# Kernel tuning notes

Measured on AMD Instinct MI355X. Metric: run time of the kernel, lower is better.

The kernel has to match this reference:

```python
import math
import jax
import jax.numpy as jnp
from jax import lax
import numpy as np

SEQ = 1024   # must be a perfect square
BSZ = 16
D = 1024     # embed_dim
NDIM = 2
SIDE = 32    # sqrt(SEQ) == one_side_length
SCALE = float(np.sqrt(1.0 / NDIM))


def setup_inputs() -> dict:
    key = jax.random.key(0)
    ks = jax.random.split(key, 8)
    x = jax.random.normal(ks[0], (SEQ, BSZ, D), dtype=jnp.float32)
    A1 = 0.2 * jax.random.normal(ks[1], (D, NDIM), dtype=jnp.float32)
    A2 = 0.2 * jax.random.normal(ks[2], (D, NDIM), dtype=jnp.float32)
    B1 = 0.2 * jax.random.normal(ks[3], (D, NDIM), dtype=jnp.float32)
    B2 = 0.2 * jax.random.normal(ks[4], (D, NDIM), dtype=jnp.float32)
    C1 = jax.random.normal(ks[5], (D, NDIM), dtype=jnp.float32)
    C2 = jax.random.normal(ks[6], (D, NDIM), dtype=jnp.float32)
    omega = jax.random.normal(ks[7], (D,), dtype=jnp.float32)
    return {"x": x, "A1": A1, "A2": A2, "B1": B1, "B2": B2,
            "C1": C1, "C2": C2, "omega": omega}


def _compute_kernel(A1, A2, B1, B2, C1, C2, n):
    """2D SSM impulse-response kernel K: (D, n, n).

    Recurrence (same math the coeff-matrix path-sum in compute_x_matrix encodes,
    cf. one_step):
      h[i,j] = a1*h[i,j-1] + a2*v[i,j-1] + b1*x[i,j]
      v[i,j] = a2*h[i-1,j] + a1*v[i-1,j] + b2*x[i,j]
      K[i,j] = <h[i,j], C1*scale> + <v[i,j], C2*scale>
    driven by a unit impulse at (0,0).
    """
    a1 = jax.nn.sigmoid(A1) * 0.5
    a2 = jax.nn.sigmoid(A2) * 0.5
    b1 = jax.nn.sigmoid(B1) * 0.5
    b2 = jax.nn.sigmoid(B2) * 0.5

    x_img = jnp.zeros((n, n), dtype=A1.dtype).at[0, 0].set(1.0)

    def row_step(carry, x_row):
        h_prev, v_prev = carry                     # (n, D, N) each
        v_row = a2 * h_prev + a1 * v_prev + b2 * x_row[:, None, None]
        # h depends on v of the PREVIOUS column in the current row
        sv = jnp.concatenate([jnp.zeros_like(v_row[:1]), v_row[:-1]], axis=0)

        def col_step(h_left, inp):
            sv_j, x_j = inp
            h_j = a1 * h_left + a2 * sv_j + b1 * x_j
            return h_j, h_j

        _, h_row = lax.scan(col_step, jnp.zeros((D, NDIM), dtype=A1.dtype),
                            (sv, x_row))
        return (h_row, v_row), (h_row, v_row)

    init = (jnp.zeros((n, D, NDIM), dtype=A1.dtype),
            jnp.zeros((n, D, NDIM), dtype=A1.dtype))
    _, (H, V) = lax.scan(row_step, init, x_img)    # (n, n, D, N)

    K = (jnp.einsum('ijdn,dn->ijd', H, C1 * SCALE)
         + jnp.einsum('ijdn,dn->ijd', V, C2 * SCALE))
    return jnp.transpose(K, (2, 0, 1))             # (D, n, n)


def reference(x, A1, A2, B1, B2, C1, C2, omega):
    seq_len, bsz, embed_dim = x.shape
    n = int(math.isqrt(seq_len))
    residual = x * omega                            # (S, B, D)

    k = _compute_kernel(A1, A2, B1, B2, C1, C2, n)  # (D, n, n)

    xi = jnp.transpose(x, (1, 2, 0)).reshape(bsz, embed_dim, n, n)
    s = (2 * n, 2 * n)
    kf = jnp.fft.rfft2(k.astype(jnp.float32), s=s)           # (D, 2n, n+1)
    xf = jnp.fft.rfft2(xi.astype(jnp.float32), s=s)          # (B, D, 2n, n+1)
    out = jnp.fft.irfft2(xf * kf, s=s)[..., :n, :n]          # (B, D, n, n)
    out = out.astype(x.dtype).reshape(bsz, embed_dim, seq_len)
    out = jnp.transpose(out, (2, 0, 1))                      # (S, B, D)
    return jax.nn.silu(out + residual)
```

## Files before the change

kernel.cpp:

```cpp
#include <hip/hip_runtime.h>
#include <math.h>

#define BSZ  16
#define DIM  1024
#define DPB  16
#define THREADS 512
#define SSTRIDE 17
#define LDSF   17472
#define LDSB   (LDSF * 4)

__device__ __forceinline__ float sigmoidf_(float v) {
    return __builtin_amdgcn_rcpf(1.0f + __expf(-v));
}

extern __shared__ float xs[];

__global__ __launch_bounds__(THREADS, 1) void ssm2d_kernel(
    const float* __restrict__ x,
    const float* __restrict__ A1, const float* __restrict__ A2,
    const float* __restrict__ B1, const float* __restrict__ B2,
    const float* __restrict__ C1, const float* __restrict__ C2,
    const float* __restrict__ omega,
    float* __restrict__ out)
{
    const int bx = blockIdx.x;
    const int b  = bx >> 6;
    const int d0 = (bx & 63) * DPB;
    const int t  = threadIdx.x;

    const int lane = t & 63;
    const int wv   = t >> 6;
    const int dd   = 2 * wv + (lane >> 5);
    const int i    = lane & 31;
    const int d    = d0 + dd;

    const float2 fA1 = *reinterpret_cast<const float2*>(A1 + 2 * d);
    const float2 fA2 = *reinterpret_cast<const float2*>(A2 + 2 * d);
    const float2 fB1 = *reinterpret_cast<const float2*>(B1 + 2 * d);
    const float2 fB2 = *reinterpret_cast<const float2*>(B2 + 2 * d);
    const float2 fC1 = *reinterpret_cast<const float2*>(C1 + 2 * d);
    const float2 fC2 = *reinterpret_cast<const float2*>(C2 + 2 * d);
    const float  om  = omega[d];

    const float a1c0 = sigmoidf_(fA1.x) * 0.5f, a1c1 = sigmoidf_(fA1.y) * 0.5f;
    const float a2c0 = sigmoidf_(fA2.x) * 0.5f, a2c1 = sigmoidf_(fA2.y) * 0.5f;
    const float b1c0 = sigmoidf_(fB1.x) * 0.5f, b1c1 = sigmoidf_(fB1.y) * 0.5f;
    const float b2c0 = sigmoidf_(fB2.x) * 0.5f, b2c1 = sigmoidf_(fB2.y) * 0.5f;
    const float sc   = 0.70710678118654752f;
    const float c1s0 = fC1.x * sc, c1s1 = fC1.y * sc;
    const float c2s0 = fC2.x * sc, c2s1 = fC2.y * sc;
    const float a1z0 = (i == 0) ? 0.f : a1c0, a1z1 = (i == 0) ? 0.f : a1c1;
    const float a2z0 = (i == 0) ? 0.f : a2c0, a2z1 = (i == 0) ? 0.f : a2c1;

    const float* xb = x + (size_t)b * DIM + d0;
    float4 L[8];
    #pragma unroll
    for (int k = 0; k < 8; ++k) {
        const int g = t + k * THREADS;
        const int s = g >> 2;
        const int q = g & 3;
        L[k] = *reinterpret_cast<const float4*>(
            xb + (size_t)s * (BSZ * DIM) + 4 * q);
    }
    #pragma unroll
    for (int k = 0; k < 8; ++k) {
        const int g = t + k * THREADS;
        const int s = g >> 2;
        const int q = g & 3;
        float* p = xs + SSTRIDE * s + 4 * q;
        p[0] = L[k].x; p[1] = L[k].y; p[2] = L[k].z; p[3] = L[k].w;
    }

    __syncthreads();

    float* rp = xs + 527 * i + dd;

    float h0 = 0.f, h1 = 0.f, v0 = 0.f, v1 = 0.f;
    float xq0 = rp[0 * SSTRIDE];
    float xq1 = rp[1 * SSTRIDE];
    float xq2 = rp[2 * SSTRIDE];

#define SSTEP(TS, XQ) do {                                                   \
        const bool  valid = ((unsigned)((TS) - i) < 32u);                    \
        const float xv    = valid ? (XQ) : 0.f;                              \
        const float t10 = b1c0 * xv, t11 = b1c1 * xv;                        \
        const float hn0 = fmaf(a1c0, h0, fmaf(a2c0, v0, t10));               \
        const float hn1 = fmaf(a1c1, h1, fmaf(a2c1, v1, t11));               \
        float vn0 = b2c0 * xv, vn1 = b2c1 * xv;                              \
        asm("s_nop 1\n\t"                                                    \
            "v_fmac_f32_dpp %0, %2, %6 wave_shr:1 row_mask:0xf bank_mask:0xf bound_ctrl:0\n\t" \
            "v_fmac_f32_dpp %1, %3, %7 wave_shr:1 row_mask:0xf bank_mask:0xf bound_ctrl:0\n\t" \
            "v_fmac_f32_dpp %0, %4, %8 wave_shr:1 row_mask:0xf bank_mask:0xf bound_ctrl:0\n\t" \
            "v_fmac_f32_dpp %1, %5, %9 wave_shr:1 row_mask:0xf bank_mask:0xf bound_ctrl:0"     \
            : "+v"(vn0), "+v"(vn1)                                           \
            : "v"(h0), "v"(h1), "v"(v0), "v"(v1),                            \
              "v"(a2z0), "v"(a2z1), "v"(a1z0), "v"(a1z1));                   \
        float y = hn0 * c1s0;                                                \
        y = fmaf(hn1, c1s1, y);                                              \
        y = fmaf(vn0, c2s0, y);                                              \
        y = fmaf(vn1, c2s1, y);                                              \
        const float z = fmaf(xv, om, y);                                     \
        const float o = z * sigmoidf_(z);                                    \
        if (valid) rp[SSTRIDE * (TS)] = o;                                   \
        h0 = hn0; h1 = hn1; v0 = vn0; v1 = vn1;                              \
    } while (0)

    #pragma unroll
    for (int ts = 0; ts < 63; ts += 3) {
        SSTEP(ts + 0, xq0); xq0 = rp[SSTRIDE * (ts + 3)];
        SSTEP(ts + 1, xq1); xq1 = rp[SSTRIDE * (ts + 4)];
        SSTEP(ts + 2, xq2); xq2 = rp[SSTRIDE * (ts + 5)];
    }
#undef SSTEP

    __syncthreads();

    float* ob = out + (size_t)b * DIM + d0;
    #pragma unroll
    for (int k = 0; k < 8; ++k) {
        const int g = t + k * THREADS;
        const int s = g >> 2;
        const int q = g & 3;
        const float* p = xs + SSTRIDE * s + 4 * q;
        float4 v;
        v.x = p[0]; v.y = p[1]; v.z = p[2]; v.w = p[3];
        *reinterpret_cast<float4*>(ob + (size_t)s * (BSZ * DIM) + 4 * q) = v;
    }
}

extern "C" void kernel_launch(void* const* d_in, const int* in_sizes, int n_in,
                              void* d_out, int out_size, void* d_ws, size_t ws_size,
                              hipStream_t stream) {
    const float* x     = (const float*)d_in[0];
    const float* A1    = (const float*)d_in[1];
    const float* A2    = (const float*)d_in[2];
    const float* B1    = (const float*)d_in[3];
    const float* B2    = (const float*)d_in[4];
    const float* C1    = (const float*)d_in[5];
    const float* C2    = (const float*)d_in[6];
    const float* omega = (const float*)d_in[7];
    float* out = (float*)d_out;

    (void)hipFuncSetAttribute(reinterpret_cast<const void*>(ssm2d_kernel),
                              hipFuncAttributeMaxDynamicSharedMemorySize, LDSB);

    dim3 grid(BSZ * (DIM / DPB));
    dim3 block(THREADS);
    hipLaunchKernelGGL(ssm2d_kernel, grid, block, LDSB, stream,
                       x, A1, A2, B1, B2, C1, C2, omega, out);
}
```

Baseline: 45.30 us.

## Run the 2D recurrence per channel in registers with one wave per block

Replaces the LDS-staged anti-diagonal wavefront, which used DPP lane shifts across 512-thread blocks, with one 64-lane wave per block in which each lane owns one channel. Each lane walks all 32x32 cells row by row, keeping the previous row's h/v state in registers, prefetching the next row of x, and writing outputs straight to global memory. This removes LDS staging, barriers, the lane-shift tricks and the invalid-step padding of the wavefront. In exchange the grid drops to 256 single-wave blocks, so each lane runs a long serial chain of 1024 cells and GPU occupancy is low. Block indices are also remapped to group channel ranges by XCD.

```diff
diff --git a/kernel.cpp b/kernel.cpp
--- a/kernel.cpp
+++ b/kernel.cpp
@@ -3,19 +3,13 @@
 
 #define BSZ  16
 #define DIM  1024
-#define DPB  16
-#define THREADS 512
-#define SSTRIDE 17
-#define LDSF   17472
-#define LDSB   (LDSF * 4)
+#define SB   (BSZ * DIM)
 
 __device__ __forceinline__ float sigmoidf_(float v) {
     return __builtin_amdgcn_rcpf(1.0f + __expf(-v));
 }
 
-extern __shared__ float xs[];
-
-__global__ __launch_bounds__(THREADS, 1) void ssm2d_kernel(
+__global__ __launch_bounds__(64, 1) void ssm2d_kernel(
     const float* __restrict__ x,
     const float* __restrict__ A1, const float* __restrict__ A2,
     const float* __restrict__ B1, const float* __restrict__ B2,
@@ -23,16 +17,13 @@
     const float* __restrict__ omega,
     float* __restrict__ out)
 {
-    const int bx = blockIdx.x;
-    const int b  = bx >> 6;
-    const int d0 = (bx & 63) * DPB;
-    const int t  = threadIdx.x;
-
-    const int lane = t & 63;
-    const int wv   = t >> 6;
-    const int dd   = 2 * wv + (lane >> 5);
-    const int i    = lane & 31;
-    const int d    = d0 + dd;
+    const int lx   = blockIdx.x;
+    const int xcd  = lx & 7;
+    const int hi   = (lx >> 3) & 1;
+    const int b    = lx >> 4;
+    const int d0   = (xcd * 2 + hi) * 64;
+    const int lane = threadIdx.x;
+    const int d    = d0 + lane;
 
     const float2 fA1 = *reinterpret_cast<const float2*>(A1 + 2 * d);
     const float2 fA2 = *reinterpret_cast<const float2*>(A2 + 2 * d);
@@ -49,83 +40,61 @@
     const float sc   = 0.70710678118654752f;
     const float c1s0 = fC1.x * sc, c1s1 = fC1.y * sc;
     const float c2s0 = fC2.x * sc, c2s1 = fC2.y * sc;
-    const float a1z0 = (i == 0) ? 0.f : a1c0, a1z1 = (i == 0) ? 0.f : a1c1;
-    const float a2z0 = (i == 0) ? 0.f : a2c0, a2z1 = (i == 0) ? 0.f : a2c1;
 
-    const float* xb = x + (size_t)b * DIM + d0;
-    float4 L[8];
+    const float* xp = x   + (size_t)b * DIM + d;
+    float*       op = out + (size_t)b * DIM + d;
+
+    float H0[32], H1[32], V0[32], V1[32];
     #pragma unroll
-    for (int k = 0; k < 8; ++k) {
-        const int g = t + k * THREADS;
-        const int s = g >> 2;
-        const int q = g & 3;
-        L[k] = *reinterpret_cast<const float4*>(
-            xb + (size_t)s * (BSZ * DIM) + 4 * q);
-    }
+    for (int j = 0; j < 32; ++j) { H0[j] = 0.f; H1[j] = 0.f; V0[j] = 0.f; V1[j] = 0.f; }
+
+    float XA[32], XB[32];
     #pragma unroll
-    for (int k = 0; k < 8; ++k) {
-        const int g = t + k * THREADS;
-        const int s = g >> 2;
-        const int q = g & 3;
-        float* p = xs + SSTRIDE * s + 4 * q;
-        p[0] = L[k].x; p[1] = L[k].y; p[2] = L[k].z; p[3] = L[k].w;
-    }
+    for (int j = 0; j < 32; ++j) XA[j] = xp[(size_t)j * SB];
 
-    __syncthreads();
-
-    float* rp = xs + 527 * i + dd;
-
-    float h0 = 0.f, h1 = 0.f, v0 = 0.f, v1 = 0.f;
-    float xq0 = rp[0 * SSTRIDE];
-    float xq1 = rp[1 * SSTRIDE];
-    float xq2 = rp[2 * SSTRIDE];
-
-#define SSTEP(TS, XQ) do {                                                   \
-        const bool  valid = ((unsigned)((TS) - i) < 32u);                    \
-        const float xv    = valid ? (XQ) : 0.f;                              \
-        const float t10 = b1c0 * xv, t11 = b1c1 * xv;                        \
-        const float hn0 = fmaf(a1c0, h0, fmaf(a2c0, v0, t10));               \
-        const float hn1 = fmaf(a1c1, h1, fmaf(a2c1, v1, t11));               \
-        float vn0 = b2c0 * xv, vn1 = b2c1 * xv;                              \
-        asm("s_nop 1\n\t"                                                    \
-            "v_fmac_f32_dpp %0, %2, %6 wave_shr:1 row_mask:0xf bank_mask:0xf bound_ctrl:0\n\t" \
-            "v_fmac_f32_dpp %1, %3, %7 wave_shr:1 row_mask:0xf bank_mask:0xf bound_ctrl:0\n\t" \
-            "v_fmac_f32_dpp %0, %4, %8 wave_shr:1 row_mask:0xf bank_mask:0xf bound_ctrl:0\n\t" \
-            "v_fmac_f32_dpp %1, %5, %9 wave_shr:1 row_mask:0xf bank_mask:0xf bound_ctrl:0"     \
-            : "+v"(vn0), "+v"(vn1)                                           \
-            : "v"(h0), "v"(h1), "v"(v0), "v"(v1),                            \
-              "v"(a2z0), "v"(a2z1), "v"(a1z0), "v"(a1z1));                   \
+#define CELL(ROW, J, XV) do {                                                \
+        const float xv  = (XV);                                              \
+        const float vn0 = fmaf(a2c0, H0[J], fmaf(a1c0, V0[J], b2c0 * xv));   \
+        const float vn1 = fmaf(a2c1, H1[J], fmaf(a1c1, V1[J], b2c1 * xv));   \
+        const float hn0 = fmaf(a1c0, hL0, fmaf(a2c0, vL0, b1c0 * xv));       \
+        const float hn1 = fmaf(a1c1, hL1, fmaf(a2c1, vL1, b1c1 * xv));       \
         float y = hn0 * c1s0;                                                \
         y = fmaf(hn1, c1s1, y);                                              \
         y = fmaf(vn0, c2s0, y);                                              \
         y = fmaf(vn1, c2s1, y);                                              \
         const float z = fmaf(xv, om, y);                                     \
-        const float o = z * sigmoidf_(z);                                    \
-        if (valid) rp[SSTRIDE * (TS)] = o;                                   \
-        h0 = hn0; h1 = hn1; v0 = vn0; v1 = vn1;                              \
+        op[(size_t)((ROW) * 32 + (J)) * SB] = z * sigmoidf_(z);              \
+        H0[J] = hn0; H1[J] = hn1; V0[J] = vn0; V1[J] = vn1;                  \
+        hL0 = hn0; hL1 = hn1; vL0 = vn0; vL1 = vn1;                          \
     } while (0)
 
-    #pragma unroll
-    for (int ts = 0; ts < 63; ts += 3) {
-        SSTEP(ts + 0, xq0); xq0 = rp[SSTRIDE * (ts + 3)];
-        SSTEP(ts + 1, xq1); xq1 = rp[SSTRIDE * (ts + 4)];
-        SSTEP(ts + 2, xq2); xq2 = rp[SSTRIDE * (ts + 5)];
+    #pragma unroll 1
+    for (int i = 0; i < 32; i += 2) {
+        {
+            float hL0 = 0.f, hL1 = 0.f, vL0 = 0.f, vL1 = 0.f;
+            #pragma unroll
+            for (int j = 0; j < 32; ++j) {
+                XB[j] = xp[(size_t)((i + 1) * 32 + j) * SB];
+                CELL(i, j, XA[j]);
+            }
+        }
+        {
+            float hL0 = 0.f, hL1 = 0.f, vL0 = 0.f, vL1 = 0.f;
+            if (i < 30) {
+                #pragma unroll
+                for (int j = 0; j < 32; ++j) {
+                    XA[j] = xp[(size_t)((i + 2) * 32 + j) * SB];
+                    CELL(i + 1, j, XB[j]);
+                }
+            } else {
+                #pragma unroll
+                for (int j = 0; j < 32; ++j) {
+                    CELL(i + 1, j, XB[j]);
+                }
+            }
+        }
     }
-#undef SSTEP
-
-    __syncthreads();
-
-    float* ob = out + (size_t)b * DIM + d0;
-    #pragma unroll
-    for (int k = 0; k < 8; ++k) {
-        const int g = t + k * THREADS;
-        const int s = g >> 2;
-        const int q = g & 3;
-        const float* p = xs + SSTRIDE * s + 4 * q;
-        float4 v;
-        v.x = p[0]; v.y = p[1]; v.z = p[2]; v.w = p[3];
-        *reinterpret_cast<float4*>(ob + (size_t)s * (BSZ * DIM) + 4 * q) = v;
-    }
+#undef CELL
 }
 
 extern "C" void kernel_launch(void* const* d_in, const int* in_sizes, int n_in,
@@ -141,11 +110,8 @@
     const float* omega = (const float*)d_in[7];
     float* out = (float*)d_out;
 
-    (void)hipFuncSetAttribute(reinterpret_cast<const void*>(ssm2d_kernel),
-                              hipFuncAttributeMaxDynamicSharedMemorySize, LDSB);
-
-    dim3 grid(BSZ * (DIM / DPB));
-    dim3 block(THREADS);
-    hipLaunchKernelGGL(ssm2d_kernel, grid, block, LDSB, stream,
+    dim3 grid(256);
+    dim3 block(64);
+    hipLaunchKernelGGL(ssm2d_kernel, grid, block, 0, stream,
                        x, A1, A2, B1, B2, C1, C2, omega, out);
 }
```

Result: slower. 74.87 us (+65.3%).
